# Kernel optimization log

Hardware: AMD Instinct MI355X
Metric: run time of the kernel (lower is better)

Reference implementation:

```python
import jax, jax.numpy as jnp
import numpy as np

B, N, C, D = 4, 8192, 3, 128


def chamfer_loss(x, y):
    # x: [B,N,3], y: [B,M,3]. Squared-distance chamfer with min-NN both ways.
    x2 = jnp.sum(x * x, axis=-1)                      # [B,N]
    y2 = jnp.sum(y * y, axis=-1)                      # [B,M]
    xy = jnp.einsum('bnc,bmc->bnm', x, y)             # [B,N,M] -- dominant 1GB buffer
    d2 = x2[:, :, None] + y2[:, None, :] - 2.0 * xy
    return jnp.mean(jnp.min(d2, axis=2)) + jnp.mean(jnp.min(d2, axis=1))


def setup_inputs() -> dict:
    key = jax.random.key(0)
    k1, k2, k3, k4 = jax.random.split(key, 4)
    return {
        'encoder_input': jax.random.normal(k1, (B, N, C), jnp.float32),
        'decoder_input': jax.random.normal(k2, (B, N, C), jnp.float32),
        'W1': jax.random.normal(k3, (C, D), jnp.float32) * 0.1,
        'b1': jnp.zeros((D,), jnp.float32),
        'W2': jax.random.normal(k4, (2 * D, C), jnp.float32) * 0.01,
        'b2': jnp.zeros((C,), jnp.float32),
    }


def reference(encoder_input, decoder_input, W1, b1, W2, b2):
    # Point-wise embedding (stand-in for the black-box DGCNN encoder)
    f_e = jax.nn.relu(encoder_input @ W1 + b1)        # [B,N,D]
    f_d = jax.nn.relu(decoder_input @ W1 + b1)        # [B,N,D]
    # Cross-set mixing (stand-in for transformer(embed_in, embed_out)),
    # concatenated with the decoder 'global_feat' as in the original.
    cross = f_d + jnp.mean(f_e, axis=1, keepdims=True)
    feat = jnp.concatenate([cross, f_d], axis=-1)     # [B,N,2D]
    displacement = feat @ W2 + b2                     # [B,N,3]
    warped = displacement + decoder_input             # warped = disp + decoder xyz
    loss1 = chamfer_loss(encoder_input, warped)       # all-pairs NN chamfer (the kernel target)
    return warped, loss1
```

## Files before the change

kernel.cpp:

```cpp
#include <hip/hip_runtime.h>
#include <hip/hip_bf16.h>
#include <hip/hip_fp16.h>
#include <float.h>

#define BB 4
#define NN 8192
#define DD 128

typedef __attribute__((ext_vector_type(8))) _Float16 f16x8;
typedef __attribute__((ext_vector_type(16))) float f32x16;
typedef __attribute__((ext_vector_type(4))) unsigned int u32x4;

__device__ __forceinline__ unsigned int pk2h(float a, float b) {
    __half2 h = __floats2half2_rn(a, b);
    return *reinterpret_cast<unsigned int*>(&h);
}


__global__ void mean_fe_kernel(const float* __restrict__ enc,
                               const float* __restrict__ W1,
                               const float* __restrict__ b1,
                               float* __restrict__ meanEp) {
    __shared__ float pts[256 * 3];
    __shared__ float red[256];
    int bid = blockIdx.x;
    int bt = bid >> 5;
    int chunk = bid & 31;
    int tid = threadIdx.x;
    int k = tid & 127;
    int half = tid >> 7;
    int base = (bt * NN + chunk * 256) * 3;
    for (int i = tid; i < 768; i += 256) pts[i] = enc[base + i];
    float w0 = W1[k], w1 = W1[128 + k], w2 = W1[256 + k], bk = b1[k];
    __syncthreads();
    float acc = 0.f;
    int p0 = half * 128;
#pragma unroll 4
    for (int i = 0; i < 128; ++i) {
        int p = (p0 + i) * 3;
        float v = pts[p] * w0 + pts[p + 1] * w1 + pts[p + 2] * w2 + bk;
        acc += fmaxf(v, 0.f);
    }
    red[tid] = acc;
    __syncthreads();
    if (tid < 128) meanEp[bid * 128 + k] = red[tid] + red[tid + 128];
}

__global__ void warp_kernel(const float* __restrict__ dec,
                            const float* __restrict__ W1,
                            const float* __restrict__ b1,
                            const float* __restrict__ W2,
                            const float* __restrict__ b2,
                            const float* __restrict__ meanEp,
                            unsigned int* __restrict__ buf,
                            float* __restrict__ out,
                            float* __restrict__ loss_slot) {
    __shared__ float sW1[384];
    __shared__ float sb1[128];
    __shared__ float sW2[768];
    __shared__ float sME[128];
    int tid = threadIdx.x;
    int idx = blockIdx.x * 256 + tid;
    int bt = idx >> 13;
    for (int i = tid; i < 384; i += 256) sW1[i] = W1[i];
    for (int i = tid; i < 768; i += 256) sW2[i] = W2[i];
    if (tid < 128) {
        sb1[tid] = b1[tid];
        float s = 0.f;
#pragma unroll 8
        for (int c = 0; c < 32; ++c) s += meanEp[(bt * 32 + c) * 128 + tid];
        sME[tid] = s;
    }
    buf[idx] = 0x7F7FFFFFu;
    buf[32768 + idx] = 0x7F7FFFFFu;
    if (idx == 0) *loss_slot = 0.f;
    __syncthreads();
    float d0 = dec[idx * 3], d1 = dec[idx * 3 + 1], d2 = dec[idx * 3 + 2];
    float a0 = 0.f, a1 = 0.f, a2 = 0.f;
    float m0 = 0.f, m1 = 0.f, m2 = 0.f;
#pragma unroll 4
    for (int k = 0; k < 128; ++k) {
        float fd = fmaxf(d0 * sW1[k] + d1 * sW1[128 + k] + d2 * sW1[256 + k] + sb1[k], 0.f);
        float wl0 = sW2[k * 3], wl1 = sW2[k * 3 + 1], wl2 = sW2[k * 3 + 2];
        float wh0 = sW2[(128 + k) * 3], wh1 = sW2[(128 + k) * 3 + 1], wh2 = sW2[(128 + k) * 3 + 2];
        a0 += fd * (wl0 + wh0);
        a1 += fd * (wl1 + wh1);
        a2 += fd * (wl2 + wh2);
        float me = sME[k];
        m0 += me * wl0; m1 += me * wl1; m2 += me * wl2;
    }
    const float invN = 1.0f / NN;
    out[idx * 3]     = a0 + m0 * invN + b2[0] + d0;
    out[idx * 3 + 1] = a1 + m1 * invN + b2[1] + d1;
    out[idx * 3 + 2] = a2 + m2 * invN + b2[2] + d2;
}

__global__ __launch_bounds__(256, 4) void chamfer_mfma_kernel(
        const float* __restrict__ enc,
        const float* __restrict__ warped,
        unsigned int* __restrict__ buf) {
    __shared__ __align__(16) union {
        unsigned int syb[1024 * 4 + 4];
        float rmin[128 * 33];
    } sh;
    __shared__ unsigned int colmin[1024];

    int bid = blockIdx.x;
    int bt = bid >> 9;
    int xc = (bid >> 3) & 63;
    int ys = bid & 7;
    int tid = threadIdx.x;
    int lane = tid & 63, wave = tid >> 6;

    int ybase = bt * NN + ys * 1024;
#pragma unroll
    for (int i = 0; i < 4; ++i) {
        int p = tid + i * 256;
        int g = (ybase + p) * 3;
        float y0 = warped[g], y1 = warped[g + 1], y2 = warped[g + 2];
        float w = y0 * y0 + y1 * y1 + y2 * y2;
        u32x4 v = { pk2h(y0, y1), pk2h(y2, 1.f), pk2h(w, 1.f), 0u };
        *reinterpret_cast<u32x4*>(&sh.syb[p * 4]) = v;
        colmin[p] = 0x7F7FFFFFu;
    }
    if (tid < 4) sh.syb[4096 + tid] = 0u;

    f16x8 afrag = {};
    int xbase = bt * NN + xc * 128 + wave * 32;
    if (lane < 32) {
        int g = (xbase + lane) * 3;
        float a = enc[g], c = enc[g + 1], e = enc[g + 2];
        float s = a * a + c * c + e * e;
        afrag[0] = (_Float16)(-2.f * a);
        afrag[1] = (_Float16)(-2.f * c);
        afrag[2] = (_Float16)(-2.f * e);
        afrag[3] = (_Float16)s;
        afrag[4] = (_Float16)1.f;
        afrag[5] = (_Float16)1.f;
    }
    __syncthreads();

    const char* base = (const char*)sh.syb + ((lane < 32) ? lane * 16 : 16384);
    int str = (lane < 32) ? 512 : 0;
    int col = lane & 31;

    float racc[16];
#pragma unroll
    for (int i = 0; i < 16; ++i) racc[i] = FLT_MAX;
    f32x16 zero = {};

    f16x8 b0 = *(const f16x8*)(base);
    f16x8 b1 = *(const f16x8*)(base + str);
#pragma unroll
    for (int t = 0; t < 16; ++t) {
        f16x8 n0 = b0, n1 = b1;
        if (t < 15) {
            n0 = *(const f16x8*)(base + (2 * t + 2) * str);
            n1 = *(const f16x8*)(base + (2 * t + 3) * str);
        }
        f32x16 q0 = __builtin_amdgcn_mfma_f32_32x32x16_f16(afrag, b0, zero, 0, 0, 0);
        f32x16 q1 = __builtin_amdgcn_mfma_f32_32x32x16_f16(afrag, b1, zero, 0, 0, 0);
#pragma unroll
        for (int i = 0; i < 16; ++i)
            racc[i] = fminf(racc[i], fminf(q0[i], q1[i]));
        float c00 = fminf(q0[0], fminf(q0[1], q0[2]));
        float c01 = fminf(q0[3], fminf(q0[4], q0[5]));
        float c02 = fminf(q0[6], fminf(q0[7], q0[8]));
        float c03 = fminf(q0[9], fminf(q0[10], q0[11]));
        float c04 = fminf(q0[12], fminf(q0[13], q0[14]));
        float cm0 = fminf(fminf(q0[15], fminf(c00, c01)), fminf(c02, fminf(c03, c04)));
        float c10 = fminf(q1[0], fminf(q1[1], q1[2]));
        float c11 = fminf(q1[3], fminf(q1[4], q1[5]));
        float c12 = fminf(q1[6], fminf(q1[7], q1[8]));
        float c13 = fminf(q1[9], fminf(q1[10], q1[11]));
        float c14 = fminf(q1[12], fminf(q1[13], q1[14]));
        float cm1 = fminf(fminf(q1[15], fminf(c10, c11)), fminf(c12, fminf(c13, c14)));
        atomicMin(&colmin[2 * t * 32 + col], __float_as_uint(cm0));
        atomicMin(&colmin[(2 * t + 1) * 32 + col], __float_as_uint(cm1));
        b0 = n0; b1 = n1;
    }

    __syncthreads();
    int half = lane >> 5;
#pragma unroll
    for (int i = 0; i < 16; ++i) {
        int row = wave * 32 + (i & 3) + 8 * (i >> 2) + 4 * half;
        sh.rmin[row * 33 + col] = racc[i];
    }
    __syncthreads();
    if (tid < 128) {
        float m = sh.rmin[tid * 33];
#pragma unroll
        for (int j = 1; j < 32; ++j) m = fminf(m, sh.rmin[tid * 33 + j]);
        atomicMin(&buf[bt * NN + xc * 128 + tid], __float_as_uint(m));
    }
#pragma unroll
    for (int i = 0; i < 4; ++i) {
        int p = tid + i * 256;
        atomicMin(&buf[32768 + bt * NN + ys * 1024 + p], colmin[p]);
    }
}

__global__ void reduce_loss_kernel(const unsigned int* __restrict__ buf,
                                   float* __restrict__ loss_slot) {
    __shared__ float red[256];
    int tid = threadIdx.x;
    int idx = blockIdx.x * 256 + tid;
    float s = 0.f;
#pragma unroll
    for (int i = 0; i < 4; ++i)
        s += __uint_as_float(buf[idx + i * 16384]);
    red[tid] = s;
    __syncthreads();
    for (int off = 128; off > 0; off >>= 1) {
        if (tid < off) red[tid] += red[tid + off];
        __syncthreads();
    }
    if (tid == 0) {
        float v = red[0] * (1.0f / (BB * NN));
        if (blockIdx.x == 0) v -= 2.0f;
        atomicAdd(loss_slot, v);
    }
}

extern "C" void kernel_launch(void* const* d_in, const int* in_sizes, int n_in,
                              void* d_out, int out_size, void* d_ws, size_t ws_size,
                              hipStream_t stream) {
    const float* enc = (const float*)d_in[0];
    const float* dec = (const float*)d_in[1];
    const float* W1  = (const float*)d_in[2];
    const float* b1  = (const float*)d_in[3];
    const float* W2  = (const float*)d_in[4];
    const float* b2  = (const float*)d_in[5];
    float* out = (float*)d_out;

    unsigned int* buf = (unsigned int*)d_ws;
    float* meanEp = (float*)((char*)d_ws + 262144);
    float* loss_slot = out + BB * NN * 3;

    mean_fe_kernel<<<BB * 32, 256, 0, stream>>>(enc, W1, b1, meanEp);
    warp_kernel<<<BB * NN / 256, 256, 0, stream>>>(dec, W1, b1, W2, b2, meanEp,
                                                   buf, out, loss_slot);
    chamfer_mfma_kernel<<<BB * 64 * 8, 256, 0, stream>>>(enc, out, buf);
    reduce_loss_kernel<<<64, 256, 0, stream>>>(buf, loss_slot);
}
```

Baseline: 46.64 us.

## Software-pipeline MFMA and replace LDS column-min atomics with per-wave arrays

The chamfer kernel now issues the MFMAs for the next step before reducing the current results, so the matrix core can overlap with the min reductions, and it prefetches B fragments two steps ahead. Column minima are no longer combined with LDS atomicMin. The two half-waves are merged with a shuffle and each wave writes its results to a private shared array, and the four per-wave arrays are min-combined before the global atomics. This removes contended LDS atomics and the colmin initialisation, at the cost of 16KB of extra shared memory, which may lower occupancy under the 4-blocks-per-CU launch bound.

```diff
diff --git a/kernel.cpp b/kernel.cpp
--- a/kernel.cpp
+++ b/kernel.cpp
@@ -95,6 +95,17 @@
     out[idx * 3 + 2] = a2 + m2 * invN + b2[2] + d2;
 }
 
+__device__ __forceinline__ float tree16(const f32x16& p) {
+    float t0 = fminf(fminf(p[0], p[1]), p[2]);
+    float t1 = fminf(fminf(p[3], p[4]), p[5]);
+    float t2 = fminf(fminf(p[6], p[7]), p[8]);
+    float t3 = fminf(fminf(p[9], p[10]), p[11]);
+    float t4 = fminf(fminf(p[12], p[13]), p[14]);
+    float r0 = fminf(fminf(t0, t1), p[15]);
+    float r1 = fminf(fminf(t2, t3), t4);
+    return fminf(r0, r1);
+}
+
 __global__ __launch_bounds__(256, 4) void chamfer_mfma_kernel(
         const float* __restrict__ enc,
         const float* __restrict__ warped,
@@ -103,7 +114,7 @@
         unsigned int syb[1024 * 4 + 4];
         float rmin[128 * 33];
     } sh;
-    __shared__ unsigned int colmin[1024];
+    __shared__ float colminW[4][1024];
 
     int bid = blockIdx.x;
     int bt = bid >> 9;
@@ -121,7 +132,6 @@
         float w = y0 * y0 + y1 * y1 + y2 * y2;
         u32x4 v = { pk2h(y0, y1), pk2h(y2, 1.f), pk2h(w, 1.f), 0u };
         *reinterpret_cast<u32x4*>(&sh.syb[p * 4]) = v;
-        colmin[p] = 0x7F7FFFFFu;
     }
     if (tid < 4) sh.syb[4096 + tid] = 0u;
 
@@ -142,62 +152,62 @@
 
     const char* base = (const char*)sh.syb + ((lane < 32) ? lane * 16 : 16384);
     int str = (lane < 32) ? 512 : 0;
-    int col = lane & 31;
 
     float racc[16];
 #pragma unroll
     for (int i = 0; i < 16; ++i) racc[i] = FLT_MAX;
     f32x16 zero = {};
 
-    f16x8 b0 = *(const f16x8*)(base);
-    f16x8 b1 = *(const f16x8*)(base + str);
+    f16x8 bC = *(const f16x8*)(base);
+    f16x8 bD = *(const f16x8*)(base + str);
+    f32x16 qa = __builtin_amdgcn_mfma_f32_32x32x16_f16(afrag, bC, zero, 0, 0, 0);
+    f32x16 qb = __builtin_amdgcn_mfma_f32_32x32x16_f16(afrag, bD, zero, 0, 0, 0);
+    bC = *(const f16x8*)(base + 2 * str);
+    bD = *(const f16x8*)(base + 3 * str);
+
 #pragma unroll
     for (int t = 0; t < 16; ++t) {
-        f16x8 n0 = b0, n1 = b1;
+        f32x16 pa = qa, pb = qb;
         if (t < 15) {
-            n0 = *(const f16x8*)(base + (2 * t + 2) * str);
-            n1 = *(const f16x8*)(base + (2 * t + 3) * str);
+            qa = __builtin_amdgcn_mfma_f32_32x32x16_f16(afrag, bC, zero, 0, 0, 0);
+            qb = __builtin_amdgcn_mfma_f32_32x32x16_f16(afrag, bD, zero, 0, 0, 0);
         }
-        f32x16 q0 = __builtin_amdgcn_mfma_f32_32x32x16_f16(afrag, b0, zero, 0, 0, 0);
-        f32x16 q1 = __builtin_amdgcn_mfma_f32_32x32x16_f16(afrag, b1, zero, 0, 0, 0);
+        if (t < 14) {
+            bC = *(const f16x8*)(base + (2 * t + 4) * str);
+            bD = *(const f16x8*)(base + (2 * t + 5) * str);
+        }
 #pragma unroll
         for (int i = 0; i < 16; ++i)
-            racc[i] = fminf(racc[i], fminf(q0[i], q1[i]));
-        float c00 = fminf(q0[0], fminf(q0[1], q0[2]));
-        float c01 = fminf(q0[3], fminf(q0[4], q0[5]));
-        float c02 = fminf(q0[6], fminf(q0[7], q0[8]));
-        float c03 = fminf(q0[9], fminf(q0[10], q0[11]));
-        float c04 = fminf(q0[12], fminf(q0[13], q0[14]));
-        float cm0 = fminf(fminf(q0[15], fminf(c00, c01)), fminf(c02, fminf(c03, c04)));
-        float c10 = fminf(q1[0], fminf(q1[1], q1[2]));
-        float c11 = fminf(q1[3], fminf(q1[4], q1[5]));
-        float c12 = fminf(q1[6], fminf(q1[7], q1[8]));
-        float c13 = fminf(q1[9], fminf(q1[10], q1[11]));
-        float c14 = fminf(q1[12], fminf(q1[13], q1[14]));
-        float cm1 = fminf(fminf(q1[15], fminf(c10, c11)), fminf(c12, fminf(c13, c14)));
-        atomicMin(&colmin[2 * t * 32 + col], __float_as_uint(cm0));
-        atomicMin(&colmin[(2 * t + 1) * 32 + col], __float_as_uint(cm1));
-        b0 = n0; b1 = n1;
-    }
-
-    __syncthreads();
-    int half = lane >> 5;
+            racc[i] = fminf(racc[i], fminf(pa[i], pb[i]));
+        float ca = tree16(pa);
+        float cb = tree16(pb);
+        ca = fminf(ca, __shfl_xor(ca, 32));
+        cb = fminf(cb, __shfl_xor(cb, 32));
+        float sel = (lane < 32) ? ca : cb;
+        colminW[wave][t * 64 + lane] = sel;
+    }
+
+    __syncthreads();
+
+    int col = lane & 31, half = lane >> 5;
 #pragma unroll
     for (int i = 0; i < 16; ++i) {
         int row = wave * 32 + (i & 3) + 8 * (i >> 2) + 4 * half;
         sh.rmin[row * 33 + col] = racc[i];
     }
+#pragma unroll
+    for (int i = 0; i < 4; ++i) {
+        int p = tid + i * 256;
+        float m = fminf(fminf(colminW[0][p], colminW[1][p]),
+                        fminf(colminW[2][p], colminW[3][p]));
+        atomicMin(&buf[32768 + bt * NN + ys * 1024 + p], __float_as_uint(m));
+    }
     __syncthreads();
     if (tid < 128) {
         float m = sh.rmin[tid * 33];
 #pragma unroll
         for (int j = 1; j < 32; ++j) m = fminf(m, sh.rmin[tid * 33 + j]);
         atomicMin(&buf[bt * NN + xc * 128 + tid], __float_as_uint(m));
-    }
-#pragma unroll
-    for (int i = 0; i < 4; ++i) {
-        int p = tid + i * 256;
-        atomicMin(&buf[32768 + bt * NN + ys * 1024 + p], colmin[p]);
     }
 }
 
```

After: 47.35 us. No clear change (+1.5%).
